# Kernel tuning notes

Measured on AMD Instinct MI355X. Metric: run time of the kernel, lower is better.

## Reference

```python
import jax, jax.numpy as jnp
import numpy as np

# Module constants from LearnableFilter.__init__
N, NB, T = 32, 2048, 1024      # N_train, N_batch, timesteps
EPS = 0.1                      # args.e_train (variation epsilon)
COUPLING = 0.5                 # args.coupling_factor
DT = 0.1
RMIN, RMAX = 1.0e5, 1.0e7
CMIN, CMAX = 1.0e-7, 1.0e-4


def setup_inputs() -> dict:
    key = jax.random.key(0)
    k0, k1, k2, k3, k4, k5, k6 = jax.random.split(key, 7)
    x = jax.random.normal(k0, (N, NB, T), dtype=jnp.float32)
    # scalar logits for R and C: rand([]) * 10 - 10
    R_ = jax.random.uniform(k1, (), dtype=jnp.float32) * 10.0 - 10.0
    C_ = jax.random.uniform(k2, (), dtype=jnp.float32) * 10.0 - 10.0
    # per-timestep multiplicative variation noise, (rand*2-1)*eps + 1
    noise_R = (jax.random.uniform(k3, (T, N, 1), dtype=jnp.float32) * 2.0 - 1.0) * EPS + 1.0
    noise_C = (jax.random.uniform(k4, (T, N, 1), dtype=jnp.float32) * 2.0 - 1.0) * EPS + 1.0
    # per-timestep coupling factor mu = rand*coupling + 1
    mu = jax.random.uniform(k5, (T, N, 1), dtype=jnp.float32) * COUPLING + 1.0
    # random initial state (random_state=True)
    memory0 = jax.random.uniform(k6, (N, NB), dtype=jnp.float32)
    return {"x": x, "R_": R_, "C_": C_, "noise_R": noise_R,
            "noise_C": noise_C, "mu": mu, "memory0": memory0}


def reference(x, R_, C_, noise_R, noise_C, mu, memory0):
    # R / C properties: sigmoid-squashed true value times multiplicative noise
    R_true = jax.nn.sigmoid(R_) * (RMAX - RMIN) + RMIN   # scalar
    C_true = jax.nn.sigmoid(C_) * (CMAX - CMIN) + CMIN   # scalar
    R = R_true * noise_R                                  # (T, N, 1)
    C = C_true * noise_C                                  # (T, N, 1)
    rc = mu * R * C                                       # (T, N, 1)
    beta = rc / (rc + DT)                                 # (T, N, 1)

    xt = jnp.transpose(x, (2, 0, 1))                      # (T, N, NB)

    def step(mem, inp):
        b, xv = inp                                       # (N,1), (N,NB)
        new = b * mem + (1.0 - b) * xv
        # torch code records memory BEFORE this step's update (last update is popped)
        return new, mem

    _, ys = jax.lax.scan(step, memory0, (beta, xt))       # ys: (T, N, NB) = [m0..m_{T-1}]
    return jnp.transpose(ys, (1, 2, 0))                   # (N, NB, T)
```

## Files before the change

kernel.cpp:

```cpp
#include <hip/hip_runtime.h>
#include <math.h>

namespace {
constexpr int N  = 32;
constexpr int NB = 2048;
constexpr int T  = 1024;
constexpr float DT_  = 0.1f;
constexpr float RMIN = 1.0e5f, RMAX = 1.0e7f;
constexpr float CMIN = 1.0e-7f, CMAX = 1.0e-4f;
constexpr int BLOCK = 1024;
constexpr int WPB   = BLOCK / 64;
constexpr int NSEG  = 4;
}

__global__ void __launch_bounds__(256)
beta_init(const float* __restrict__ Rp, const float* __restrict__ Cp,
          const float* __restrict__ noise_R, const float* __restrict__ noise_C,
          const float* __restrict__ mu, float* __restrict__ betaT)
{
    const int i = blockIdx.x * 256 + threadIdx.x;
    const float R_true = (RMAX - RMIN) / (1.0f + expf(-Rp[0])) + RMIN;
    const float C_true = (CMAX - CMIN) / (1.0f + expf(-Cp[0])) + CMIN;
    const float rc = mu[i] * (R_true * noise_R[i]) * (C_true * noise_C[i]);
    const int t = i >> 5, n = i & (N - 1);
    betaT[n * T + t] = rc / (rc + DT_);
}

__global__ void __launch_bounds__(BLOCK, 8)
lf_scan(const float* __restrict__ x,
        const float* __restrict__ betaT,
        const float* __restrict__ memory0,
        float* __restrict__ out)
{
    __shared__ __align__(16) float beta_s[T];
    const int tid = threadIdx.x;
    const int n   = blockIdx.y;

    beta_s[tid] = betaT[n * T + tid];
    __syncthreads();

    const int w    = tid >> 6;
    const int lane = tid & 63;
    const int nb   = blockIdx.x * WPB + w;

    const size_t base = ((size_t)n * NB + (size_t)nb) * (size_t)T;
    const float4* __restrict__ xv = reinterpret_cast<const float4*>(x + base);
    float4*       __restrict__ ov = reinterpret_cast<float4*>(out + base);
    const float4* __restrict__ bv = reinterpret_cast<const float4*>(beta_s);

    float4 X[NSEG];
    #pragma unroll
    for (int s = 0; s < NSEG; ++s) X[s] = xv[s * 64 + lane];

    float P[NSEG], Q[NSEG];
    #pragma unroll
    for (int s = 0; s < NSEG; ++s) {
        const float4 b  = bv[s * 64 + lane];
        const float4 xc = X[s];
        float p = b.x, q = (1.0f - b.x) * xc.x;
        q = fmaf(b.y, q, (1.0f - b.y) * xc.y); p *= b.y;
        q = fmaf(b.z, q, (1.0f - b.z) * xc.z); p *= b.z;
        q = fmaf(b.w, q, (1.0f - b.w) * xc.w); p *= b.w;
        P[s] = p; Q[s] = q;
    }

    #pragma unroll
    for (int d = 1; d < 64; d <<= 1) {
        float Pin[NSEG], Qin[NSEG];
        #pragma unroll
        for (int s = 0; s < NSEG; ++s) {
            Pin[s] = __shfl_up(P[s], (unsigned)d, 64);
            Qin[s] = __shfl_up(Q[s], (unsigned)d, 64);
        }
        #pragma unroll
        for (int s = 0; s < NSEG; ++s) {
            if (lane >= d) {
                Q[s] = fmaf(P[s], Qin[s], Q[s]);
                P[s] = P[s] * Pin[s];
            }
        }
    }

    float ms = memory0[n * NB + nb];
    #pragma unroll
    for (int s = 0; s < NSEG; ++s) {
        const float Pe  = __shfl_up(P[s], 1u, 64);
        const float Qe  = __shfl_up(Q[s], 1u, 64);
        const float P63 = __shfl(P[s], 63, 64);
        const float Q63 = __shfl(Q[s], 63, 64);
        float me = (lane == 0) ? ms : fmaf(Pe, ms, Qe);

        const float4 b  = bv[s * 64 + lane];
        const float4 xc = X[s];
        float4 o;
        o.x = me; me = fmaf(b.x, me - xc.x, xc.x);
        o.y = me; me = fmaf(b.y, me - xc.y, xc.y);
        o.z = me; me = fmaf(b.z, me - xc.z, xc.z);
        o.w = me;
        ov[s * 64 + lane] = o;

        ms = fmaf(P63, ms, Q63);
    }
}

extern "C" void kernel_launch(void* const* d_in, const int* in_sizes, int n_in,
                              void* d_out, int out_size, void* d_ws, size_t ws_size,
                              hipStream_t stream) {
    const float* x   = (const float*)d_in[0];
    const float* Rp  = (const float*)d_in[1];
    const float* Cp  = (const float*)d_in[2];
    const float* nR  = (const float*)d_in[3];
    const float* nC  = (const float*)d_in[4];
    const float* muv = (const float*)d_in[5];
    const float* m0  = (const float*)d_in[6];
    float* out   = (float*)d_out;
    float* betaT = (float*)d_ws;

    beta_init<<<dim3((T * N) / 256), 256, 0, stream>>>(Rp, Cp, nR, nC, muv, betaT);
    dim3 grid(NB / WPB, N);
    lf_scan<<<grid, BLOCK, 0, stream>>>(x, betaT, m0, out);
}
```

Before: 111.4 us.

## Drop LDS beta staging, use 256-thread blocks and nontemporal x/out accesses

The scan kernel no longer stages beta in shared memory behind a barrier. Each wave now reads beta directly from global memory, where it should be cached, and keeps it in registers. Blocks shrink from 1024 to 256 threads on a 1D grid, which should improve scheduling flexibility. Loads of x and stores of out use nontemporal hints to avoid polluting cache on this purely streaming kernel, at the cost of extra global beta reads per wave.

```diff
diff --git a/kernel.cpp b/kernel.cpp
--- a/kernel.cpp
+++ b/kernel.cpp
@@ -8,9 +8,9 @@
 constexpr float DT_  = 0.1f;
 constexpr float RMIN = 1.0e5f, RMAX = 1.0e7f;
 constexpr float CMIN = 1.0e-7f, CMAX = 1.0e-4f;
-constexpr int BLOCK = 1024;
-constexpr int WPB   = BLOCK / 64;
-constexpr int NSEG  = 4;
+constexpr int NSEG = 4;
+
+typedef float f4 __attribute__((ext_vector_type(4)));
 }
 
 __global__ void __launch_bounds__(256)
@@ -26,37 +26,35 @@
     betaT[n * T + t] = rc / (rc + DT_);
 }
 
-__global__ void __launch_bounds__(BLOCK, 8)
+__global__ void __launch_bounds__(256, 8)
 lf_scan(const float* __restrict__ x,
         const float* __restrict__ betaT,
         const float* __restrict__ memory0,
         float* __restrict__ out)
 {
-    __shared__ __align__(16) float beta_s[T];
-    const int tid = threadIdx.x;
-    const int n   = blockIdx.y;
-
-    beta_s[tid] = betaT[n * T + tid];
-    __syncthreads();
-
+    const int tid  = threadIdx.x;
     const int w    = tid >> 6;
     const int lane = tid & 63;
-    const int nb   = blockIdx.x * WPB + w;
+    const int bid  = blockIdx.x;
+    const int n    = bid >> 9;
+    const int nb   = ((bid & 511) << 2) + w;
 
     const size_t base = ((size_t)n * NB + (size_t)nb) * (size_t)T;
-    const float4* __restrict__ xv = reinterpret_cast<const float4*>(x + base);
-    float4*       __restrict__ ov = reinterpret_cast<float4*>(out + base);
-    const float4* __restrict__ bv = reinterpret_cast<const float4*>(beta_s);
+    const f4* __restrict__ xv = reinterpret_cast<const f4*>(x + base);
+    f4*       __restrict__ ov = reinterpret_cast<f4*>(out + base);
+    const f4* __restrict__ bv = reinterpret_cast<const f4*>(betaT + n * T);
 
-    float4 X[NSEG];
+    f4 X[NSEG], B[NSEG];
     #pragma unroll
-    for (int s = 0; s < NSEG; ++s) X[s] = xv[s * 64 + lane];
+    for (int s = 0; s < NSEG; ++s) X[s] = __builtin_nontemporal_load(&xv[s * 64 + lane]);
+    #pragma unroll
+    for (int s = 0; s < NSEG; ++s) B[s] = bv[s * 64 + lane];
 
     float P[NSEG], Q[NSEG];
     #pragma unroll
     for (int s = 0; s < NSEG; ++s) {
-        const float4 b  = bv[s * 64 + lane];
-        const float4 xc = X[s];
+        const f4 b  = B[s];
+        const f4 xc = X[s];
         float p = b.x, q = (1.0f - b.x) * xc.x;
         q = fmaf(b.y, q, (1.0f - b.y) * xc.y); p *= b.y;
         q = fmaf(b.z, q, (1.0f - b.z) * xc.z); p *= b.z;
@@ -90,14 +88,14 @@
         const float Q63 = __shfl(Q[s], 63, 64);
         float me = (lane == 0) ? ms : fmaf(Pe, ms, Qe);
 
-        const float4 b  = bv[s * 64 + lane];
-        const float4 xc = X[s];
-        float4 o;
+        const f4 b  = B[s];
+        const f4 xc = X[s];
+        f4 o;
         o.x = me; me = fmaf(b.x, me - xc.x, xc.x);
         o.y = me; me = fmaf(b.y, me - xc.y, xc.y);
         o.z = me; me = fmaf(b.z, me - xc.z, xc.z);
         o.w = me;
-        ov[s * 64 + lane] = o;
+        __builtin_nontemporal_store(o, &ov[s * 64 + lane]);
 
         ms = fmaf(P63, ms, Q63);
     }
@@ -117,6 +115,5 @@
     float* betaT = (float*)d_ws;
 
     beta_init<<<dim3((T * N) / 256), 256, 0, stream>>>(Rp, Cp, nR, nC, muv, betaT);
-    dim3 grid(NB / WPB, N);
-    lf_scan<<<grid, BLOCK, 0, stream>>>(x, betaT, m0, out);
+    lf_scan<<<dim3(N * (NB / 4)), 256, 0, stream>>>(x, betaT, m0, out);
 }
```

Measured after the change: 96.01 us. 13.8% less time.
